# Kernel optimization log

Hardware: AMD Instinct MI355X
Metric: run time of the kernel (lower is better)

## Reference

```python
import jax, jax.numpy as jnp
import numpy as np
import math

B, S, D = 16, 4096, 64

def setup_inputs() -> dict:
    key = jax.random.key(0)
    kq, kk, kv = jax.random.split(key, 3)
    query = jax.random.normal(kq, (B, S, D), dtype=jnp.float32)
    k_ = jax.random.normal(kk, (B, S, D), dtype=jnp.float32)
    value = jax.random.normal(kv, (B, S, D), dtype=jnp.float32)
    # causal mask: 1 = allowed, 0 = masked (set to -inf), broadcast over batch
    mask = jnp.tril(jnp.ones((S, S), dtype=jnp.int32))[None, :, :]
    return {"query": query, "key": k_, "value": value, "mask": mask, "key_dim": D}

def reference(query, key, value, mask, key_dim):
    # scores: [B, S, S] = Q @ K^T / sqrt(dk)
    scores = jnp.einsum('bqd,bkd->bqk', query, key) / math.sqrt(key_dim)
    scores = jnp.where(mask == 0, -jnp.inf, scores)
    attn = jax.nn.softmax(scores, axis=-1)
    return jnp.einsum('bqk,bkd->bqd', attn, value)
```

## Files before the change

### kernel.cpp

```cpp
#include <hip/hip_runtime.h>

typedef _Float16 half8 __attribute__((ext_vector_type(8)));
typedef float f32x4 __attribute__((ext_vector_type(4)));

union Frag { half8 v; unsigned int u32[4]; uint4 u4; };
union Pack4 { _Float16 h[4]; uint2 u; };

constexpr int S = 4096;
constexpr int D = 64;
constexpr int NB = 16;
constexpr int LTS = 72;

__global__ __launch_bounds__(256)
void prep_kernel(const float* __restrict__ K, const float* __restrict__ V,
                 _Float16* __restrict__ K16, _Float16* __restrict__ VT) {
    __shared__ float tl[64 * 66];
    const int tid = threadIdx.x;
    const int s0 = blockIdx.x * 64;
    const int b  = blockIdx.y;
    const float* Kb = K + ((size_t)b * S + s0) * D;
    const float* Vb = V + ((size_t)b * S + s0) * D;
    _Float16* K16b = K16 + ((size_t)b * S + s0) * D;

    #pragma unroll
    for (int i = 0; i < 2; ++i) {
        int e8 = tid + 256 * i;
        float4 a = ((const float4*)Kb)[2 * e8];
        float4 c = ((const float4*)Kb)[2 * e8 + 1];
        Frag f;
        f.v[0]=(_Float16)a.x; f.v[1]=(_Float16)a.y; f.v[2]=(_Float16)a.z; f.v[3]=(_Float16)a.w;
        f.v[4]=(_Float16)c.x; f.v[5]=(_Float16)c.y; f.v[6]=(_Float16)c.z; f.v[7]=(_Float16)c.w;
        ((uint4*)K16b)[e8] = f.u4;
    }
    #pragma unroll
    for (int i = 0; i < 4; ++i) {
        int fi = tid + 256 * i;
        int r = fi >> 4, c4 = (fi & 15) << 2;
        float4 v = *(const float4*)(Vb + (size_t)r * D + c4);
        float2* p = (float2*)&tl[r * 66 + c4];
        p[0] = make_float2(v.x, v.y);
        p[1] = make_float2(v.z, v.w);
    }
    __syncthreads();
    _Float16* VTb = VT + (size_t)b * D * S;
    #pragma unroll
    for (int i = 0; i < 2; ++i) {
        int fi = tid + 256 * i;
        int d = fi >> 3, s8 = (fi & 7) << 3;
        Frag f;
        #pragma unroll
        for (int j = 0; j < 8; ++j) f.v[j] = (_Float16)tl[(s8 + j) * 66 + d];
        *(uint4*)(VTb + (size_t)d * S + s0 + s8) = f.u4;
    }
}

__global__ __launch_bounds__(256, 4)
void fattn_kernel(const float* __restrict__ Q, const _Float16* __restrict__ K16,
                  const _Float16* __restrict__ VT16, float* __restrict__ Out) {
    __shared__ __align__(16) _Float16 kt[64 * LTS];
    __shared__ __align__(16) _Float16 vt[64 * LTS];
    __shared__ __align__(16) _Float16 pt[4 * 16 * LTS];

    const int tid  = threadIdx.x;
    const int wave = tid >> 6;
    const int lane = tid & 63;
    const int ln   = lane & 15;
    const int quad = lane >> 4;

    const int bx = blockIdx.x;
    const int b  = bx & 15;
    const int qt = 63 - (bx >> 4);

    const float* Qb = Q + (size_t)b * S * D;
    const _Float16* Kb = K16 + (size_t)b * S * D;
    const _Float16* VTb = VT16 + (size_t)b * D * S;
    float* Ob = Out + (size_t)b * S * D;

    const float qscale = 0.125f * 1.44269504088896340736f;
    const int qrow_base = qt * 64 + wave * 16;

    Frag qf[2];
    {
        const float* qrow = Qb + (size_t)(qrow_base + ln) * D + quad * 8;
        #pragma unroll
        for (int ks = 0; ks < 2; ++ks) {
            float4 a = *(const float4*)(qrow + ks * 32);
            float4 c = *(const float4*)(qrow + ks * 32 + 4);
            Frag f;
            f.v[0]=(_Float16)(a.x*qscale); f.v[1]=(_Float16)(a.y*qscale);
            f.v[2]=(_Float16)(a.z*qscale); f.v[3]=(_Float16)(a.w*qscale);
            f.v[4]=(_Float16)(c.x*qscale); f.v[5]=(_Float16)(c.y*qscale);
            f.v[6]=(_Float16)(c.z*qscale); f.v[7]=(_Float16)(c.w*qscale);
            qf[ks] = f;
        }
    }

    f32x4 o[4] = {};
    float l_acc = 0.f;
    _Float16* ptw = pt + wave * 16 * LTS;

    for (int t = 0; t <= qt; ++t) {
        const int k0 = t * 64;
        __syncthreads();

        #pragma unroll
        for (int i = 0; i < 2; ++i) {
            int fi = tid + 256 * i;
            int r = fi >> 3, c8 = (fi & 7) << 3;
            uint4 kk = *(const uint4*)(Kb + (size_t)(k0 + r) * D + c8);
            uint4 vv = *(const uint4*)(VTb + (size_t)r * S + k0 + c8);
            *(uint4*)(kt + r * LTS + c8) = kk;
            *(uint4*)(vt + r * LTS + c8) = vv;
        }
        __syncthreads();

        #pragma unroll
        for (int ct = 0; ct < 4; ++ct) {
            Frag kf0, kf1;
            kf0.u4 = *(const uint4*)(kt + (ct * 16 + ln) * LTS + quad * 8);
            kf1.u4 = *(const uint4*)(kt + (ct * 16 + ln) * LTS + 32 + quad * 8);
            f32x4 acc = {0.f, 0.f, 0.f, 0.f};
            acc = __builtin_amdgcn_mfma_f32_16x16x32_f16(kf0.v, qf[0].v, acc, 0, 0, 0);
            acc = __builtin_amdgcn_mfma_f32_16x16x32_f16(kf1.v, qf[1].v, acc, 0, 0, 0);
            if (t == qt) {
                int keyb = k0 + ct * 16 + quad * 4;
                int qrow = qrow_base + ln;
                #pragma unroll
                for (int r = 0; r < 4; ++r)
                    if (keyb + r > qrow) acc[r] = -1e30f;
            }
            Pack4 pk;
            float psum = 0.f;
            #pragma unroll
            for (int r = 0; r < 4; ++r) {
                float p = exp2f(acc[r]);
                psum += p;
                pk.h[r] = (_Float16)p;
            }
            l_acc += psum;
            *(uint2*)(ptw + ln * LTS + ct * 16 + quad * 4) = pk.u;
        }

        Frag pf[2];
        #pragma unroll
        for (int ks = 0; ks < 2; ++ks)
            pf[ks].u4 = *(const uint4*)(ptw + ln * LTS + ks * 32 + quad * 8);

        #pragma unroll
        for (int ks = 0; ks < 2; ++ks) {
            #pragma unroll
            for (int sub = 0; sub < 4; ++sub) {
                Frag vf;
                vf.u4 = *(const uint4*)(vt + (sub * 16 + ln) * LTS + ks * 32 + quad * 8);
                o[sub] = __builtin_amdgcn_mfma_f32_16x16x32_f16(pf[ks].v, vf.v, o[sub], 0, 0, 0);
            }
        }
    }

    float lf = l_acc;
    lf += __shfl_xor(lf, 16, 64);
    lf += __shfl_xor(lf, 32, 64);
    #pragma unroll
    for (int r = 0; r < 4; ++r) {
        float lrow = __shfl(lf, quad * 4 + r, 64);
        float inv = 1.0f / lrow;
        #pragma unroll
        for (int sub = 0; sub < 4; ++sub) {
            Ob[(size_t)(qrow_base + quad * 4 + r) * D + sub * 16 + ln] =
                o[sub][r] * inv;
        }
    }
}

extern "C" void kernel_launch(void* const* d_in, const int* in_sizes, int n_in,
                              void* d_out, int out_size, void* d_ws, size_t ws_size,
                              hipStream_t stream) {
    const float* Q = (const float*)d_in[0];
    const float* K = (const float*)d_in[1];
    const float* V = (const float*)d_in[2];
    float* O = (float*)d_out;

    _Float16* K16 = (_Float16*)d_ws;
    _Float16* VT16 = (_Float16*)((char*)d_ws + (size_t)NB * S * D * 2);

    hipLaunchKernelGGL(prep_kernel, dim3(S / 64, NB), dim3(256), 0, stream, K, V, K16, VT16);
    hipLaunchKernelGGL(fattn_kernel, dim3(64 * NB), dim3(256), 0, stream, Q, K16, VT16, O);
}
```

Measured before the change: 206.9 us.

## Double-buffer K/V LDS tiles with register prefetch of the next tile

The K and V^T shared-memory tiles are now double-buffered. The next tile's global loads are issued into registers before the current tile's QK^T, softmax and PV work, and are written to the alternate LDS buffer afterwards. This removes one __syncthreads per iteration and hides global-load latency behind MFMA work. In exchange, LDS use per block rises to about 46KB, and launch bounds drop from 4 to 3 blocks per CU, which lowers occupancy and adds register pressure from the prefetch buffers.

```diff
diff --git a/kernel.cpp b/kernel.cpp
--- a/kernel.cpp
+++ b/kernel.cpp
@@ -54,11 +54,11 @@
     }
 }
 
-__global__ __launch_bounds__(256, 4)
+__global__ __launch_bounds__(256, 3)
 void fattn_kernel(const float* __restrict__ Q, const _Float16* __restrict__ K16,
                   const _Float16* __restrict__ VT16, float* __restrict__ Out) {
-    __shared__ __align__(16) _Float16 kt[64 * LTS];
-    __shared__ __align__(16) _Float16 vt[64 * LTS];
+    __shared__ __align__(16) _Float16 kt[2][64 * LTS];
+    __shared__ __align__(16) _Float16 vt[2][64 * LTS];
     __shared__ __align__(16) _Float16 pt[4 * 16 * LTS];
 
     const int tid  = threadIdx.x;
@@ -78,6 +78,9 @@
 
     const float qscale = 0.125f * 1.44269504088896340736f;
     const int qrow_base = qt * 64 + wave * 16;
+
+    const int sr0 = tid >> 3;
+    const int sc8 = (tid & 7) << 3;
 
     Frag qf[2];
     {
@@ -99,26 +102,43 @@
     float l_acc = 0.f;
     _Float16* ptw = pt + wave * 16 * LTS;
 
+    uint4 kk[2], vv[2];
+    #pragma unroll
+    for (int i = 0; i < 2; ++i) {
+        int r = sr0 + 32 * i;
+        kk[i] = *(const uint4*)(Kb + (size_t)r * D + sc8);
+        vv[i] = *(const uint4*)(VTb + (size_t)r * S + sc8);
+    }
+    #pragma unroll
+    for (int i = 0; i < 2; ++i) {
+        int r = sr0 + 32 * i;
+        *(uint4*)(kt[0] + r * LTS + sc8) = kk[i];
+        *(uint4*)(vt[0] + r * LTS + sc8) = vv[i];
+    }
+
     for (int t = 0; t <= qt; ++t) {
         const int k0 = t * 64;
         __syncthreads();
 
-        #pragma unroll
-        for (int i = 0; i < 2; ++i) {
-            int fi = tid + 256 * i;
-            int r = fi >> 3, c8 = (fi & 7) << 3;
-            uint4 kk = *(const uint4*)(Kb + (size_t)(k0 + r) * D + c8);
-            uint4 vv = *(const uint4*)(VTb + (size_t)r * S + k0 + c8);
-            *(uint4*)(kt + r * LTS + c8) = kk;
-            *(uint4*)(vt + r * LTS + c8) = vv;
-        }
-        __syncthreads();
+        const _Float16* ktc = kt[t & 1];
+        const _Float16* vtc = vt[t & 1];
+
+        const bool pre = (t < qt);
+        if (pre) {
+            const int k0n = k0 + 64;
+            #pragma unroll
+            for (int i = 0; i < 2; ++i) {
+                int r = sr0 + 32 * i;
+                kk[i] = *(const uint4*)(Kb + (size_t)(k0n + r) * D + sc8);
+                vv[i] = *(const uint4*)(VTb + (size_t)r * S + k0n + sc8);
+            }
+        }
 
         #pragma unroll
         for (int ct = 0; ct < 4; ++ct) {
             Frag kf0, kf1;
-            kf0.u4 = *(const uint4*)(kt + (ct * 16 + ln) * LTS + quad * 8);
-            kf1.u4 = *(const uint4*)(kt + (ct * 16 + ln) * LTS + 32 + quad * 8);
+            kf0.u4 = *(const uint4*)(ktc + (ct * 16 + ln) * LTS + quad * 8);
+            kf1.u4 = *(const uint4*)(ktc + (ct * 16 + ln) * LTS + 32 + quad * 8);
             f32x4 acc = {0.f, 0.f, 0.f, 0.f};
             acc = __builtin_amdgcn_mfma_f32_16x16x32_f16(kf0.v, qf[0].v, acc, 0, 0, 0);
             acc = __builtin_amdgcn_mfma_f32_16x16x32_f16(kf1.v, qf[1].v, acc, 0, 0, 0);
@@ -151,8 +171,19 @@
             #pragma unroll
             for (int sub = 0; sub < 4; ++sub) {
                 Frag vf;
-                vf.u4 = *(const uint4*)(vt + (sub * 16 + ln) * LTS + ks * 32 + quad * 8);
+                vf.u4 = *(const uint4*)(vtc + (sub * 16 + ln) * LTS + ks * 32 + quad * 8);
                 o[sub] = __builtin_amdgcn_mfma_f32_16x16x32_f16(pf[ks].v, vf.v, o[sub], 0, 0, 0);
+            }
+        }
+
+        if (pre) {
+            _Float16* ktn = kt[(t + 1) & 1];
+            _Float16* vtn = vt[(t + 1) & 1];
+            #pragma unroll
+            for (int i = 0; i < 2; ++i) {
+                int r = sr0 + 32 * i;
+                *(uint4*)(ktn + r * LTS + sc8) = kk[i];
+                *(uint4*)(vtn + r * LTS + sc8) = vv[i];
             }
         }
     }
```

Result: slower. 245.9 us (+18.8%).
